# Kernel optimization log

Measured on AMD Instinct MI355X. Metric: run time of the kernel, lower is better.

The kernel has to match this reference:

```python
import jax, jax.numpy as jnp
import numpy as np


def _conv(x, k, pad):
    # x: [B,1,H,W], k: [1,1,kh,kw]
    return jax.lax.conv_general_dilated(
        x, k, window_strides=(1, 1), padding=[(pad, pad), (pad, pad)],
        dimension_numbers=('NCHW', 'OIHW', 'NCHW'))


def _gauss_kernel(size=15, sigma=2.0):
    c = np.arange(size, dtype=np.float32) - size // 2
    k = np.exp(-(c[:, None] ** 2 + c[None, :] ** 2) / (2.0 * sigma ** 2))
    k = k / k.sum()
    return jnp.asarray(k, dtype=jnp.float32)[None, None]


_SOBEL_X = jnp.array([[[[-1., 0., 1.], [-2., 0., 2.], [-1., 0., 1.]]]], dtype=jnp.float32)
_SOBEL_Y = jnp.array([[[[-1., -2., -1.], [0., 0., 0.], [1., 2., 1.]]]], dtype=jnp.float32)
_GAUSS = _gauss_kernel(15, 2.0)


def _edge_density(img):
    gray = 0.299 * img[:, 0] + 0.587 * img[:, 1] + 0.114 * img[:, 2]  # [B,H,W]
    box = jnp.ones((1, 1, 5, 5), jnp.float32) / 25.0  # avg_pool2d, count_include_pad
    blurred = _conv(gray[:, None], box, 2)
    gx = _conv(blurred, _SOBEL_X, 1)
    gy = _conv(blurred, _SOBEL_Y, 1)
    mag = jnp.sqrt(gx ** 2 + gy ** 2)
    hi = mag.max() * 0.2
    lo = hi * 0.3
    edge_map = ((mag > lo) & (mag < hi)).astype(jnp.float32)
    return _conv(edge_map, _GAUSS, 7)  # [B,1,H,W]


def _color_sparsity(img):
    # Replaces the O(K*B*H*W) python loop over unique quantized colors with a
    # 32^3-bin histogram (scatter-add) and a single per-pixel gather.
    b, c, h, w = img.shape
    idx = jnp.clip(jnp.round(img * 31.0), 0, 31).astype(jnp.int32)  # [B,3,H,W]
    code = idx[:, 0] * 1024 + idx[:, 1] * 32 + idx[:, 2]  # [B,H,W]
    counts = jnp.zeros(32 * 32 * 32, jnp.float32).at[code.reshape(-1)].add(1.0)
    prob = counts[code] / float(b * h * w)  # [B,H,W]
    return (-jnp.log(prob + 1e-9) * 1.5)[:, None]  # [B,1,H,W]


def setup_inputs() -> dict:
    key = jax.random.key(0)
    img = jax.random.uniform(key, (1, 3, 3072, 3072), dtype=jnp.float32)
    return {
        'img': img,
        'alpha': jnp.asarray(0.5, dtype=jnp.float32),
        'beta': jnp.asarray(0.5, dtype=jnp.float32),
    }


def reference(img, alpha, beta):
    ed = _edge_density(img)
    cs = _color_sparsity(img)
    en = (ed - ed.min()) / (ed.max() - ed.min() + 1e-9)
    cn = (cs - cs.min()) / (cs.max() - cs.min() + 1e-9)
    return jax.nn.sigmoid(alpha * en + beta * cn)  # [B,1,H,W]
```

## Files before the change

### kernel.cpp

```cpp
#include <hip/hip_runtime.h>
#include <math.h>

#define TW 3072
#define TH 3072
#define NPIX (TW*TH)

__device__ __forceinline__ int qcode(float r, float g, float b) {
    int ir = min(max((int)rintf(__fmul_rn(r, 31.f)), 0), 31);
    int ig = min(max((int)rintf(__fmul_rn(g, 31.f)), 0), 31);
    int ib = min(max((int)rintf(__fmul_rn(b, 31.f)), 0), 31);
    return ir * 1024 + ig * 32 + ib;
}

__device__ __forceinline__ float grayf(float r, float g, float b) {
    return __fadd_rn(__fadd_rn(__fmul_rn(0.299f, r), __fmul_rn(0.587f, g)),
                     __fmul_rn(0.114f, b));
}

__global__ __launch_bounds__(1024) void k_pre(const float4* __restrict__ img4,
                                              float4* __restrict__ gray4,
                                              ushort4* __restrict__ code4,
                                              unsigned* __restrict__ parthist,
                                              unsigned* __restrict__ scal) {
    if (blockIdx.x == 0 && threadIdx.x == 0) {
        scal[0] = 0u;
        scal[1] = 0x7F800000u;
        scal[2] = 0u;
        scal[3] = 0u;
        scal[4] = 0xFFFFFFFFu;
    }
    __shared__ unsigned lh[16384];
    for (int t = threadIdx.x; t < 16384; t += 1024) lh[t] = 0u;
    __syncthreads();
    const int total4 = NPIX / 4;
    const int stride = 256 * 1024;
    int base = blockIdx.x * 1024 + threadIdx.x;
    float4 rn = img4[base], gn = img4[base + total4], bn = img4[base + 2 * total4];
#pragma unroll
    for (int k = 0; k < 9; k++) {
        int p = base + k * stride;
        float4 r = rn, g = gn, b = bn;
        if (k < 8) {
            int pn = p + stride;
            rn = img4[pn]; gn = img4[pn + total4]; bn = img4[pn + 2 * total4];
        }
        float4 gy;
        gy.x = grayf(r.x, g.x, b.x); gy.y = grayf(r.y, g.y, b.y);
        gy.z = grayf(r.z, g.z, b.z); gy.w = grayf(r.w, g.w, b.w);
        gray4[p] = gy;
        int c0 = qcode(r.x, g.x, b.x), c1 = qcode(r.y, g.y, b.y);
        int c2 = qcode(r.z, g.z, b.z), c3 = qcode(r.w, g.w, b.w);
        atomicAdd(&lh[c0 >> 1], (c0 & 1) ? 0x10000u : 1u);
        atomicAdd(&lh[c1 >> 1], (c1 & 1) ? 0x10000u : 1u);
        atomicAdd(&lh[c2 >> 1], (c2 & 1) ? 0x10000u : 1u);
        atomicAdd(&lh[c3 >> 1], (c3 & 1) ? 0x10000u : 1u);
        ushort4 cc;
        cc.x = (unsigned short)c0; cc.y = (unsigned short)c1;
        cc.z = (unsigned short)c2; cc.w = (unsigned short)c3;
        code4[p] = cc;
    }
    __syncthreads();
    unsigned* dst = parthist + (size_t)blockIdx.x * 16384;
    for (int t = threadIdx.x; t < 16384; t += 1024) dst[t] = lh[t];
}

__device__ __forceinline__ void blockMaxMinAtomic(float vmax, float vmin,
                                                  unsigned* pmax, unsigned* pmin) {
#pragma unroll
    for (int o = 32; o > 0; o >>= 1) {
        vmax = fmaxf(vmax, __shfl_down(vmax, o));
        vmin = fminf(vmin, __shfl_down(vmin, o));
    }
    __shared__ float smax[8], smin[8];
    int lane = threadIdx.x & 63, wv = threadIdx.x >> 6;
    if (lane == 0) { smax[wv] = vmax; smin[wv] = vmin; }
    __syncthreads();
    if (threadIdx.x == 0) {
        int nw = blockDim.x >> 6;
        float a = smax[0], b = smin[0];
        for (int k = 1; k < nw; k++) { a = fmaxf(a, smax[k]); b = fminf(b, smin[k]); }
        if (pmax) atomicMax(pmax, __float_as_uint(a));
        if (pmin) atomicMin(pmin, __float_as_uint(b));
    }
}

#define BS_W 256
#define BS_H 24
#define GTW 264
#define GTH 30
#define BLW 260
#define BLH 26
#define NCONV ((TW/BS_W)*(TH/BS_H))
__global__ __launch_bounds__(512) void k_boxsobel(const float* __restrict__ g,
                                                  float* __restrict__ mag,
                                                  unsigned* __restrict__ scal,
                                                  const unsigned* __restrict__ parthist,
                                                  float* __restrict__ cstab) {
    __shared__ float smem[GTH * GTW + BLH * BLW];
    int tid = threadIdx.x;
    int bid = blockIdx.x;

    if (bid >= NCONV) {
        unsigned* slo = (unsigned*)smem;
        unsigned* shi = slo + 512;
        int rbid = bid - NCONV;
        int tsub = tid >> 6;
        int pl = tid & 63;
        int b = rbid * 64 + pl;
        unsigned lo = 0u, hi = 0u;
#pragma unroll 8
        for (int j = 0; j < 32; j++) {
            unsigned v = parthist[(size_t)(tsub * 32 + j) * 16384 + b];
            lo += v & 0xFFFFu;
            hi += v >> 16;
        }
        slo[tid] = lo;
        shi[tid] = hi;
        __syncthreads();
        if (tid < 64) {
            unsigned Lo = 0u, Hi = 0u;
#pragma unroll
            for (int t = 0; t < 8; t++) { Lo += slo[t * 64 + tid]; Hi += shi[t * 64 + tid]; }
            const float N = (float)NPIX;
            int bb = rbid * 64 + tid;
            cstab[2 * bb]     = -logf((float)Lo / N + 1e-9f) * 1.5f;
            cstab[2 * bb + 1] = -logf((float)Hi / N + 1e-9f) * 1.5f;
            unsigned mx = max(Lo, Hi);
            unsigned mn = 0xFFFFFFFFu;
            if (Lo) mn = Lo;
            if (Hi) mn = min(mn, Hi);
#pragma unroll
            for (int o = 32; o > 0; o >>= 1) {
                mx = max(mx, (unsigned)__shfl_down((int)mx, o));
                mn = min(mn, (unsigned)__shfl_down((int)mn, o));
            }
            if (tid == 0) { atomicMax(&scal[3], mx); atomicMin(&scal[4], mn); }
        }
        return;
    }

    float* GT = smem;
    float* BL = smem + GTH * GTW;
    int x0 = (bid % (TW / BS_W)) * BS_W;
    int y0 = (bid / (TW / BS_W)) * BS_H;
    {
        float tmp[16];
#pragma unroll
        for (int u = 0; u < 16; u++) {
            int t = tid + u * 512;
            int ly = t / GTW, lx = t - ly * GTW;
            int y = y0 - 3 + ly, x = x0 - 3 + lx;
            bool in = (t < GTH * GTW) && ((unsigned)y < TH) && ((unsigned)x < TW);
            tmp[u] = in ? g[(size_t)y * TW + x] : 0.f;
        }
#pragma unroll
        for (int u = 0; u < 16; u++) {
            int t = tid + u * 512;
            if (t < GTH * GTW) GT[t] = tmp[u];
        }
    }
    __syncthreads();
    for (int t = tid; t < BLH * 65; t += 512) {
        int by = t / 65, gx = t - by * 65;
        int c0 = gx * 4;
        float acc[4] = {0.f, 0.f, 0.f, 0.f};
#pragma unroll
        for (int a = 0; a < 5; a++) {
            const float* rp = &GT[(by + a) * GTW + c0];
            float4 A = *(const float4*)rp;
            float4 B = *(const float4*)(rp + 4);
            float v[8] = {A.x, A.y, A.z, A.w, B.x, B.y, B.z, B.w};
#pragma unroll
            for (int j = 0; j < 4; j++)
#pragma unroll
                for (int b = 0; b < 5; b++)
                    acc[j] = __fadd_rn(acc[j], __fmul_rn(v[j + b], 0.04f));
        }
        int yb = y0 - 1 + by;
        float4 o;
        float* ov = (float*)&o;
#pragma unroll
        for (int j = 0; j < 4; j++) {
            int xb = x0 - 1 + c0 + j;
            ov[j] = ((unsigned)yb < TH && (unsigned)xb < TW) ? acc[j] : 0.f;
        }
        *(float4*)&BL[by * BLW + c0] = o;
    }
    __syncthreads();
    float tmax = 0.f;
    for (int t = tid; t < BS_H * 64; t += 512) {
        int oy = t >> 6, gx = t & 63;
        int c0 = gx * 4;
        float v[3][6];
#pragma unroll
        for (int a = 0; a < 3; a++) {
            const float* rp = &BL[(oy + a) * BLW + c0];
            float4 P = *(const float4*)rp;
            float2 Q = *(const float2*)(rp + 4);
            v[a][0] = P.x; v[a][1] = P.y; v[a][2] = P.z; v[a][3] = P.w;
            v[a][4] = Q.x; v[a][5] = Q.y;
        }
        float4 mo;
        float* mv = (float*)&mo;
#pragma unroll
        for (int j = 0; j < 4; j++) {
            float gxv = 0.f;
            gxv = __fadd_rn(gxv, __fmul_rn(-1.f, v[0][j + 0]));
            gxv = __fadd_rn(gxv, v[0][j + 2]);
            gxv = __fadd_rn(gxv, __fmul_rn(-2.f, v[1][j + 0]));
            gxv = __fadd_rn(gxv, __fmul_rn(2.f, v[1][j + 2]));
            gxv = __fadd_rn(gxv, __fmul_rn(-1.f, v[2][j + 0]));
            gxv = __fadd_rn(gxv, v[2][j + 2]);
            float gyv = 0.f;
            gyv = __fadd_rn(gyv, __fmul_rn(-1.f, v[0][j + 0]));
            gyv = __fadd_rn(gyv, __fmul_rn(-2.f, v[0][j + 1]));
            gyv = __fadd_rn(gyv, __fmul_rn(-1.f, v[0][j + 2]));
            gyv = __fadd_rn(gyv, v[2][j + 0]);
            gyv = __fadd_rn(gyv, __fmul_rn(2.f, v[2][j + 1]));
            gyv = __fadd_rn(gyv, v[2][j + 2]);
            float m = sqrtf(__fadd_rn(__fmul_rn(gxv, gxv), __fmul_rn(gyv, gyv)));
            mv[j] = m;
            tmax = fmaxf(tmax, m);
        }
        *(float4*)&mag[(size_t)(y0 + oy) * TW + x0 + c0] = mo;
    }
    blockMaxMinAtomic(tmax, 0.f, &scal[0], nullptr);
}

#define GS_W 256
#define GS_H 48
#define E_H 62
#define EWB 10
__global__ __launch_bounds__(512) void k_gauss(const float* __restrict__ mag,
                                               float* __restrict__ ed,
                                               const unsigned* __restrict__ scal,
                                               unsigned* __restrict__ scalw) {
    __shared__ float wt[15];
    __shared__ unsigned E8[E_H * EWB];
    __shared__ float EH[E_H * GS_W];
    if (threadIdx.x == 0) {
        float w[15];
        float s = 0.f;
        for (int t = 0; t < 15; t++) {
            int c = t - 7;
            w[t] = expf(-(float)(c * c) * 0.125f);
            s += w[t];
        }
        for (int t = 0; t < 15; t++) wt[t] = w[t] / s;
    }
    __syncthreads();
    float magmax = __uint_as_float(scal[0]);
    float hi = __fmul_rn(magmax, 0.2f);
    float lo = __fmul_rn(hi, 0.3f);
    int tid = threadIdx.x;
    int lane = tid & 63, wave = tid >> 6;
    int x0 = blockIdx.x * GS_W;
    int y0 = blockIdx.y * GS_H;
    for (int item0 = wave * 5; item0 < E_H * 5; item0 += 40) {
        float mv5[5];
#pragma unroll
        for (int u = 0; u < 5; u++) {
            int item = item0 + u;
            int ly = item / 5, ch = item - ly * 5;
            int y = y0 - 7 + ly;
            int lx = ch * 64 + lane;
            int x = x0 - 7 + lx;
            mv5[u] = ((unsigned)y < TH && lx < 270 && (unsigned)x < TW)
                         ? mag[(size_t)y * TW + x] : 0.f;
        }
#pragma unroll
        for (int u = 0; u < 5; u++) {
            int item = item0 + u;
            int ly = item / 5, ch = item - ly * 5;
            unsigned long long mask = __ballot(mv5[u] > lo && mv5[u] < hi);
            if (lane < 2) E8[ly * EWB + ch * 2 + lane] = (unsigned)(mask >> (32 * lane));
        }
    }
    __syncthreads();
    for (int t = tid; t < E_H * 64; t += 512) {
        int ly = t >> 6, gx = t & 63;
        int c0 = gx * 4;
        int w0 = c0 >> 5, sh = c0 & 31;
        unsigned lo32 = E8[ly * EWB + w0];
        unsigned hi32 = E8[ly * EWB + w0 + 1];
        unsigned long long win = (((unsigned long long)hi32 << 32) | lo32) >> sh;
        float e[18];
#pragma unroll
        for (int j = 0; j < 18; j++) e[j] = (float)((unsigned)(win >> j) & 1u);
        float4 o;
        float* ov = (float*)&o;
#pragma unroll
        for (int j = 0; j < 4; j++) {
            float acc = 0.f;
#pragma unroll
            for (int k = 0; k < 15; k++) acc = fmaf(e[j + k], wt[k], acc);
            ov[j] = acc;
        }
        *(float4*)&EH[ly * GS_W + c0] = o;
    }
    __syncthreads();
    float tmin = INFINITY, tmax = 0.f;
    {
        int c0 = lane * 4;
        int r0 = wave * 6;
        float acc[6][4];
#pragma unroll
        for (int s = 0; s < 6; s++) {
            acc[s][0] = 0.f; acc[s][1] = 0.f; acc[s][2] = 0.f; acc[s][3] = 0.f;
        }
#pragma unroll
        for (int j = 0; j < 20; j++) {
            float4 v = *(const float4*)&EH[(r0 + j) * GS_W + c0];
#pragma unroll
            for (int s = 0; s < 6; s++) {
                int k = j - s;
                if (k >= 0 && k < 15) {
                    acc[s][0] = fmaf(v.x, wt[k], acc[s][0]);
                    acc[s][1] = fmaf(v.y, wt[k], acc[s][1]);
                    acc[s][2] = fmaf(v.z, wt[k], acc[s][2]);
                    acc[s][3] = fmaf(v.w, wt[k], acc[s][3]);
                }
            }
        }
#pragma unroll
        for (int s = 0; s < 6; s++) {
            float4 o;
            o.x = acc[s][0]; o.y = acc[s][1]; o.z = acc[s][2]; o.w = acc[s][3];
            *(float4*)&ed[(size_t)(y0 + r0 + s) * TW + x0 + c0] = o;
            tmin = fminf(tmin, fminf(fminf(o.x, o.y), fminf(o.z, o.w)));
            tmax = fmaxf(tmax, fmaxf(fmaxf(o.x, o.y), fmaxf(o.z, o.w)));
        }
    }
    blockMaxMinAtomic(tmax, tmin, &scalw[2], &scalw[1]);
}

__global__ __launch_bounds__(1024) void k_final(float4* __restrict__ io4,
                                                const ushort4* __restrict__ code4,
                                                const float* __restrict__ cstab,
                                                const unsigned* __restrict__ scal,
                                                const float* __restrict__ alphap,
                                                const float* __restrict__ betap) {
    __shared__ unsigned short cnS[32768];
    const float N = (float)NPIX;
    float csmin = -logf((float)scal[3] / N + 1e-9f) * 1.5f;
    float csmax = -logf((float)scal[4] / N + 1e-9f) * 1.5f;
    float csrange = csmax - csmin + 1e-9f;
    {
        float4 cv[8];
#pragma unroll
        for (int u = 0; u < 8; u++)
            cv[u] = ((const float4*)cstab)[threadIdx.x + u * 1024];
        unsigned* cnS32 = (unsigned*)cnS;
#pragma unroll
        for (int u = 0; u < 8; u++) {
            int t4 = threadIdx.x + u * 1024;
            float vv[4] = {cv[u].x, cv[u].y, cv[u].z, cv[u].w};
            unsigned q[4];
#pragma unroll
            for (int j = 0; j < 4; j++) {
                float cn = (vv[j] - csmin) / csrange;
                int qi = (int)rintf(cn * 65535.f);
                q[j] = (unsigned)min(max(qi, 0), 65535);
            }
            cnS32[2 * t4]     = q[0] | (q[1] << 16);
            cnS32[2 * t4 + 1] = q[2] | (q[3] << 16);
        }
    }
    float edmin = __uint_as_float(scal[1]);
    float edmax = __uint_as_float(scal[2]);
    float edrange = edmax - edmin + 1e-9f;
    float alpha = *alphap, beta = *betap;
    const int half = NPIX / 8;
    int p0 = blockIdx.x * 1024 + threadIdx.x;
    int p1 = p0 + half;
    float4 e0 = io4[p0]; ushort4 cc0 = code4[p0];
    float4 e1 = io4[p1]; ushort4 cc1 = code4[p1];
    __syncthreads();
    {
        float edv[4] = {e0.x, e0.y, e0.z, e0.w};
        unsigned short cv[4] = {cc0.x, cc0.y, cc0.z, cc0.w};
        float ov[4];
#pragma unroll
        for (int t = 0; t < 4; t++) {
            float en = (edv[t] - edmin) / edrange;
            float cn = (float)cnS[cv[t]] * (1.f / 65535.f);
            float x = alpha * en + beta * cn;
            ov[t] = 1.f / (1.f + expf(-x));
        }
        float4 o; o.x = ov[0]; o.y = ov[1]; o.z = ov[2]; o.w = ov[3];
        io4[p0] = o;
    }
    {
        float edv[4] = {e1.x, e1.y, e1.z, e1.w};
        unsigned short cv[4] = {cc1.x, cc1.y, cc1.z, cc1.w};
        float ov[4];
#pragma unroll
        for (int t = 0; t < 4; t++) {
            float en = (edv[t] - edmin) / edrange;
            float cn = (float)cnS[cv[t]] * (1.f / 65535.f);
            float x = alpha * en + beta * cn;
            ov[t] = 1.f / (1.f + expf(-x));
        }
        float4 o; o.x = ov[0]; o.y = ov[1]; o.z = ov[2]; o.w = ov[3];
        io4[p1] = o;
    }
}

extern "C" void kernel_launch(void* const* d_in, const int* in_sizes, int n_in,
                              void* d_out, int out_size, void* d_ws, size_t ws_size,
                              hipStream_t stream) {
    const float* img = (const float*)d_in[0];
    const float* alphap = (const float*)d_in[1];
    const float* betap = (const float*)d_in[2];
    float* out = (float*)d_out;

    char* ws = (char*)d_ws;
    unsigned* scal = (unsigned*)ws;
    float* cstab = (float*)(ws + 1024 + 131072);
    float* G = (float*)(ws + 524288);
    float* M = (float*)(ws + 524288 + (size_t)NPIX * 4);
    unsigned short* code = (unsigned short*)(ws + 524288 + (size_t)NPIX * 8);
    unsigned* parthist = (unsigned*)M;
    parthist = (unsigned*)(ws + 524288 + (size_t)NPIX * 10);

    hipLaunchKernelGGL(k_pre, dim3(256), dim3(1024), 0, stream,
                       (const float4*)img, (float4*)G, (ushort4*)code, parthist, scal);
    hipLaunchKernelGGL(k_boxsobel, dim3(NCONV + 256), dim3(512), 0, stream,
                       G, M, scal, parthist, cstab);
    hipLaunchKernelGGL(k_gauss, dim3(TW / GS_W, TH / GS_H), dim3(512), 0, stream,
                       M, out, scal, scal);
    hipLaunchKernelGGL(k_final, dim3(1152), dim3(1024), 0, stream, (float4*)out,
                       (const ushort4*)code, cstab, scal, alphap, betap);
}
```

Measured before the change: 296.5 us.

## Move histogram build into conv kernel and reduction into gauss kernel

The shared-memory histogram leaves the gray/quantize pre-pass, which becomes a light streaming kernel. Histogram blocks that re-read the stored colour codes are interleaved (one in seven) with the box/Sobel blocks, and the partial-histogram reduction is interleaved (one in four) with the Gaussian blocks. The final kernel becomes a grid-stride loop over 512 blocks. The aim is to take the atomic-heavy histogram off the critical path and overlap it with the convolution work, at the cost of re-reading the code buffer and using 64KB of dynamic shared memory in the conv kernel.

```diff
diff --git a/kernel.cpp b/kernel.cpp
--- a/kernel.cpp
+++ b/kernel.cpp
@@ -17,10 +17,9 @@
                      __fmul_rn(0.114f, b));
 }
 
-__global__ __launch_bounds__(1024) void k_pre(const float4* __restrict__ img4,
+__global__ __launch_bounds__(256) void k_gray(const float4* __restrict__ img4,
                                               float4* __restrict__ gray4,
                                               ushort4* __restrict__ code4,
-                                              unsigned* __restrict__ parthist,
                                               unsigned* __restrict__ scal) {
     if (blockIdx.x == 0 && threadIdx.x == 0) {
         scal[0] = 0u;
@@ -29,39 +28,34 @@
         scal[3] = 0u;
         scal[4] = 0xFFFFFFFFu;
     }
-    __shared__ unsigned lh[16384];
-    for (int t = threadIdx.x; t < 16384; t += 1024) lh[t] = 0u;
-    __syncthreads();
     const int total4 = NPIX / 4;
-    const int stride = 256 * 1024;
-    int base = blockIdx.x * 1024 + threadIdx.x;
-    float4 rn = img4[base], gn = img4[base + total4], bn = img4[base + 2 * total4];
-#pragma unroll
-    for (int k = 0; k < 9; k++) {
-        int p = base + k * stride;
-        float4 r = rn, g = gn, b = bn;
-        if (k < 8) {
-            int pn = p + stride;
-            rn = img4[pn]; gn = img4[pn + total4]; bn = img4[pn + 2 * total4];
-        }
-        float4 gy;
-        gy.x = grayf(r.x, g.x, b.x); gy.y = grayf(r.y, g.y, b.y);
-        gy.z = grayf(r.z, g.z, b.z); gy.w = grayf(r.w, g.w, b.w);
-        gray4[p] = gy;
-        int c0 = qcode(r.x, g.x, b.x), c1 = qcode(r.y, g.y, b.y);
-        int c2 = qcode(r.z, g.z, b.z), c3 = qcode(r.w, g.w, b.w);
-        atomicAdd(&lh[c0 >> 1], (c0 & 1) ? 0x10000u : 1u);
-        atomicAdd(&lh[c1 >> 1], (c1 & 1) ? 0x10000u : 1u);
-        atomicAdd(&lh[c2 >> 1], (c2 & 1) ? 0x10000u : 1u);
-        atomicAdd(&lh[c3 >> 1], (c3 & 1) ? 0x10000u : 1u);
-        ushort4 cc;
+    const int gstride = 2304 * 256;
+    int t0 = blockIdx.x * 256 + threadIdx.x;
+#pragma unroll
+    for (int k = 0; k < 4; k += 2) {
+        int p = t0 + k * gstride;
+        int q = p + gstride;
+        float4 r0 = img4[p], g0 = img4[p + total4], b0 = img4[p + 2 * total4];
+        float4 r1 = img4[q], g1 = img4[q + total4], b1 = img4[q + 2 * total4];
+        float4 gy0, gy1;
+        gy0.x = grayf(r0.x, g0.x, b0.x); gy0.y = grayf(r0.y, g0.y, b0.y);
+        gy0.z = grayf(r0.z, g0.z, b0.z); gy0.w = grayf(r0.w, g0.w, b0.w);
+        gy1.x = grayf(r1.x, g1.x, b1.x); gy1.y = grayf(r1.y, g1.y, b1.y);
+        gy1.z = grayf(r1.z, g1.z, b1.z); gy1.w = grayf(r1.w, g1.w, b1.w);
+        gray4[p] = gy0;
+        gray4[q] = gy1;
+        int c0 = qcode(r0.x, g0.x, b0.x), c1 = qcode(r0.y, g0.y, b0.y);
+        int c2 = qcode(r0.z, g0.z, b0.z), c3 = qcode(r0.w, g0.w, b0.w);
+        int d0 = qcode(r1.x, g1.x, b1.x), d1 = qcode(r1.y, g1.y, b1.y);
+        int d2 = qcode(r1.z, g1.z, b1.z), d3 = qcode(r1.w, g1.w, b1.w);
+        ushort4 cc, dd;
         cc.x = (unsigned short)c0; cc.y = (unsigned short)c1;
         cc.z = (unsigned short)c2; cc.w = (unsigned short)c3;
+        dd.x = (unsigned short)d0; dd.y = (unsigned short)d1;
+        dd.z = (unsigned short)d2; dd.w = (unsigned short)d3;
         code4[p] = cc;
-    }
-    __syncthreads();
-    unsigned* dst = parthist + (size_t)blockIdx.x * 16384;
-    for (int t = threadIdx.x; t < 16384; t += 1024) dst[t] = lh[t];
+        code4[q] = dd;
+    }
 }
 
 __device__ __forceinline__ void blockMaxMinAtomic(float vmax, float vmin,
@@ -90,59 +84,52 @@
 #define GTH 30
 #define BLW 260
 #define BLH 26
-#define NCONV ((TW/BS_W)*(TH/BS_H))
-__global__ __launch_bounds__(512) void k_boxsobel(const float* __restrict__ g,
+#define NCONV1 ((TW/BS_W)*(TH/BS_H))
+__global__ __launch_bounds__(512) void k_convhist(const float* __restrict__ g,
                                                   float* __restrict__ mag,
                                                   unsigned* __restrict__ scal,
-                                                  const unsigned* __restrict__ parthist,
-                                                  float* __restrict__ cstab) {
-    __shared__ float smem[GTH * GTW + BLH * BLW];
+                                                  const uint4* __restrict__ codeq,
+                                                  unsigned* __restrict__ parthist) {
+    extern __shared__ char dsm[];
     int tid = threadIdx.x;
     int bid = blockIdx.x;
 
-    if (bid >= NCONV) {
-        unsigned* slo = (unsigned*)smem;
-        unsigned* shi = slo + 512;
-        int rbid = bid - NCONV;
-        int tsub = tid >> 6;
-        int pl = tid & 63;
-        int b = rbid * 64 + pl;
-        unsigned lo = 0u, hi = 0u;
-#pragma unroll 8
-        for (int j = 0; j < 32; j++) {
-            unsigned v = parthist[(size_t)(tsub * 32 + j) * 16384 + b];
-            lo += v & 0xFFFFu;
-            hi += v >> 16;
-        }
-        slo[tid] = lo;
-        shi[tid] = hi;
+    if (bid % 7 == 6) {
+        unsigned* lh = (unsigned*)dsm;
+        int hbid = bid / 7;
+        for (int t = tid; t < 16384; t += 512) lh[t] = 0u;
         __syncthreads();
-        if (tid < 64) {
-            unsigned Lo = 0u, Hi = 0u;
-#pragma unroll
-            for (int t = 0; t < 8; t++) { Lo += slo[t * 64 + tid]; Hi += shi[t * 64 + tid]; }
-            const float N = (float)NPIX;
-            int bb = rbid * 64 + tid;
-            cstab[2 * bb]     = -logf((float)Lo / N + 1e-9f) * 1.5f;
-            cstab[2 * bb + 1] = -logf((float)Hi / N + 1e-9f) * 1.5f;
-            unsigned mx = max(Lo, Hi);
-            unsigned mn = 0xFFFFFFFFu;
-            if (Lo) mn = Lo;
-            if (Hi) mn = min(mn, Hi);
-#pragma unroll
-            for (int o = 32; o > 0; o >>= 1) {
-                mx = max(mx, (unsigned)__shfl_down((int)mx, o));
-                mn = min(mn, (unsigned)__shfl_down((int)mn, o));
-            }
-            if (tid == 0) { atomicMax(&scal[3], mx); atomicMin(&scal[4], mn); }
-        }
+        const int cbase = hbid * 4608;
+        uint4 w[9];
+#pragma unroll
+        for (int r = 0; r < 9; r++) w[r] = codeq[cbase + r * 512 + tid];
+#pragma unroll
+        for (int r = 0; r < 9; r++) {
+            unsigned v;
+            v = w[r].x;
+            { unsigned c = v & 0xFFFFu; atomicAdd(&lh[c >> 1], (c & 1) ? 0x10000u : 1u); }
+            { unsigned c = v >> 16;     atomicAdd(&lh[c >> 1], (c & 1) ? 0x10000u : 1u); }
+            v = w[r].y;
+            { unsigned c = v & 0xFFFFu; atomicAdd(&lh[c >> 1], (c & 1) ? 0x10000u : 1u); }
+            { unsigned c = v >> 16;     atomicAdd(&lh[c >> 1], (c & 1) ? 0x10000u : 1u); }
+            v = w[r].z;
+            { unsigned c = v & 0xFFFFu; atomicAdd(&lh[c >> 1], (c & 1) ? 0x10000u : 1u); }
+            { unsigned c = v >> 16;     atomicAdd(&lh[c >> 1], (c & 1) ? 0x10000u : 1u); }
+            v = w[r].w;
+            { unsigned c = v & 0xFFFFu; atomicAdd(&lh[c >> 1], (c & 1) ? 0x10000u : 1u); }
+            { unsigned c = v >> 16;     atomicAdd(&lh[c >> 1], (c & 1) ? 0x10000u : 1u); }
+        }
+        __syncthreads();
+        unsigned* dst = parthist + (size_t)hbid * 16384;
+        for (int t = tid; t < 16384; t += 512) dst[t] = lh[t];
         return;
     }
 
-    float* GT = smem;
-    float* BL = smem + GTH * GTW;
-    int x0 = (bid % (TW / BS_W)) * BS_W;
-    int y0 = (bid / (TW / BS_W)) * BS_H;
+    int cidx = bid - bid / 7;
+    float* GT = (float*)dsm;
+    float* BL = GT + GTH * GTW;
+    int x0 = (cidx % (TW / BS_W)) * BS_W;
+    int y0 = (cidx / (TW / BS_W)) * BS_H;
     {
         float tmp[16];
 #pragma unroll
@@ -231,13 +218,58 @@
 #define GS_H 48
 #define E_H 62
 #define EWB 10
-__global__ __launch_bounds__(512) void k_gauss(const float* __restrict__ mag,
-                                               float* __restrict__ ed,
-                                               const unsigned* __restrict__ scal,
-                                               unsigned* __restrict__ scalw) {
+__global__ __launch_bounds__(512) void k_gaussred(const float* __restrict__ mag,
+                                                  float* __restrict__ ed,
+                                                  unsigned* __restrict__ scal,
+                                                  const unsigned* __restrict__ parthist,
+                                                  float* __restrict__ cstab) {
     __shared__ float wt[15];
     __shared__ unsigned E8[E_H * EWB];
     __shared__ float EH[E_H * GS_W];
+    __shared__ unsigned slo[512], shi[512];
+    int tid = threadIdx.x;
+    int bid = blockIdx.x;
+
+    if ((bid & 3) == 3) {
+        int rbid = bid >> 2;
+        int tsub = tid >> 6;
+        int pl = tid & 63;
+        int b = rbid * 64 + pl;
+        unsigned lo = 0u, hi = 0u;
+#pragma unroll 8
+        for (int j = 0; j < 32; j++) {
+            unsigned v = parthist[(size_t)(tsub * 32 + j) * 16384 + b];
+            lo += v & 0xFFFFu;
+            hi += v >> 16;
+        }
+        slo[tid] = lo;
+        shi[tid] = hi;
+        __syncthreads();
+        if (tid < 64) {
+            unsigned Lo = 0u, Hi = 0u;
+#pragma unroll
+            for (int t = 0; t < 8; t++) { Lo += slo[t * 64 + tid]; Hi += shi[t * 64 + tid]; }
+            const float N = (float)NPIX;
+            int bb = rbid * 64 + tid;
+            cstab[2 * bb]     = -logf((float)Lo / N + 1e-9f) * 1.5f;
+            cstab[2 * bb + 1] = -logf((float)Hi / N + 1e-9f) * 1.5f;
+            unsigned mx = max(Lo, Hi);
+            unsigned mn = 0xFFFFFFFFu;
+            if (Lo) mn = Lo;
+            if (Hi) mn = min(mn, Hi);
+#pragma unroll
+            for (int o = 32; o > 0; o >>= 1) {
+                mx = max(mx, (unsigned)__shfl_down((int)mx, o));
+                mn = min(mn, (unsigned)__shfl_down((int)mn, o));
+            }
+            if (tid == 0) { atomicMax(&scal[3], mx); atomicMin(&scal[4], mn); }
+        }
+        return;
+    }
+
+    int cidx = bid - (bid >> 2);
+    int x0 = (cidx % (TW / GS_W)) * GS_W;
+    int y0 = (cidx / (TW / GS_W)) * GS_H;
     if (threadIdx.x == 0) {
         float w[15];
         float s = 0.f;
@@ -252,10 +284,7 @@
     float magmax = __uint_as_float(scal[0]);
     float hi = __fmul_rn(magmax, 0.2f);
     float lo = __fmul_rn(hi, 0.3f);
-    int tid = threadIdx.x;
     int lane = tid & 63, wave = tid >> 6;
-    int x0 = blockIdx.x * GS_W;
-    int y0 = blockIdx.y * GS_H;
     for (int item0 = wave * 5; item0 < E_H * 5; item0 += 40) {
         float mv5[5];
 #pragma unroll
@@ -331,7 +360,7 @@
             tmax = fmaxf(tmax, fmaxf(fmaxf(o.x, o.y), fmaxf(o.z, o.w)));
         }
     }
-    blockMaxMinAtomic(tmax, tmin, &scalw[2], &scalw[1]);
+    blockMaxMinAtomic(tmax, tmin, &scal[2], &scal[1]);
 }
 
 __global__ __launch_bounds__(1024) void k_final(float4* __restrict__ io4,
@@ -370,15 +399,14 @@
     float edmax = __uint_as_float(scal[2]);
     float edrange = edmax - edmin + 1e-9f;
     float alpha = *alphap, beta = *betap;
-    const int half = NPIX / 8;
-    int p0 = blockIdx.x * 1024 + threadIdx.x;
-    int p1 = p0 + half;
-    float4 e0 = io4[p0]; ushort4 cc0 = code4[p0];
-    float4 e1 = io4[p1]; ushort4 cc1 = code4[p1];
-    __syncthreads();
-    {
-        float edv[4] = {e0.x, e0.y, e0.z, e0.w};
-        unsigned short cv[4] = {cc0.x, cc0.y, cc0.z, cc0.w};
+    __syncthreads();
+    const int total4 = NPIX / 4;
+    int stride = gridDim.x * blockDim.x;
+    for (int p = blockIdx.x * blockDim.x + threadIdx.x; p < total4; p += stride) {
+        float4 edv4 = io4[p];
+        ushort4 cc = code4[p];
+        float edv[4] = {edv4.x, edv4.y, edv4.z, edv4.w};
+        unsigned short cv[4] = {cc.x, cc.y, cc.z, cc.w};
         float ov[4];
 #pragma unroll
         for (int t = 0; t < 4; t++) {
@@ -387,22 +415,9 @@
             float x = alpha * en + beta * cn;
             ov[t] = 1.f / (1.f + expf(-x));
         }
-        float4 o; o.x = ov[0]; o.y = ov[1]; o.z = ov[2]; o.w = ov[3];
-        io4[p0] = o;
-    }
-    {
-        float edv[4] = {e1.x, e1.y, e1.z, e1.w};
-        unsigned short cv[4] = {cc1.x, cc1.y, cc1.z, cc1.w};
-        float ov[4];
-#pragma unroll
-        for (int t = 0; t < 4; t++) {
-            float en = (edv[t] - edmin) / edrange;
-            float cn = (float)cnS[cv[t]] * (1.f / 65535.f);
-            float x = alpha * en + beta * cn;
-            ov[t] = 1.f / (1.f + expf(-x));
-        }
-        float4 o; o.x = ov[0]; o.y = ov[1]; o.z = ov[2]; o.w = ov[3];
-        io4[p1] = o;
+        float4 o;
+        o.x = ov[0]; o.y = ov[1]; o.z = ov[2]; o.w = ov[3];
+        io4[p] = o;
     }
 }
 
@@ -420,15 +435,14 @@
     float* G = (float*)(ws + 524288);
     float* M = (float*)(ws + 524288 + (size_t)NPIX * 4);
     unsigned short* code = (unsigned short*)(ws + 524288 + (size_t)NPIX * 8);
-    unsigned* parthist = (unsigned*)M;
-    parthist = (unsigned*)(ws + 524288 + (size_t)NPIX * 10);
-
-    hipLaunchKernelGGL(k_pre, dim3(256), dim3(1024), 0, stream,
-                       (const float4*)img, (float4*)G, (ushort4*)code, parthist, scal);
-    hipLaunchKernelGGL(k_boxsobel, dim3(NCONV + 256), dim3(512), 0, stream,
-                       G, M, scal, parthist, cstab);
-    hipLaunchKernelGGL(k_gauss, dim3(TW / GS_W, TH / GS_H), dim3(512), 0, stream,
-                       M, out, scal, scal);
-    hipLaunchKernelGGL(k_final, dim3(1152), dim3(1024), 0, stream, (float4*)out,
+    unsigned* parthist = (unsigned*)(ws + 524288 + (size_t)NPIX * 10);
+
+    hipLaunchKernelGGL(k_gray, dim3(2304), dim3(256), 0, stream,
+                       (const float4*)img, (float4*)G, (ushort4*)code, scal);
+    hipLaunchKernelGGL(k_convhist, dim3(7 * 256), dim3(512), 65536, stream,
+                       G, M, scal, (const uint4*)code, parthist);
+    hipLaunchKernelGGL(k_gaussred, dim3(1024), dim3(512), 0, stream,
+                       M, out, scal, parthist, cstab);
+    hipLaunchKernelGGL(k_final, dim3(512), dim3(1024), 0, stream, (float4*)out,
                        (const ushort4*)code, cstab, scal, alphap, betap);
 }
```

Result: faster. 284.9 us (-3.9%).
